# Kernel tuning notes

Measured on AMD Instinct MI355X. Metric: run time of the kernel, lower is better.

## Reference

```python
import jax, jax.numpy as jnp
import numpy as np

DIM_Q = 512
DIM_K = 512
DIM_V = 512
NUM_HEADS = 8
TEMPERATURE = 0.1
LN_EPS = 1e-5


def setup_inputs() -> dict:
    key = jax.random.key(0)
    ks = jax.random.split(key, 12)
    B, n_q, n_k = 8, 1024, 1024
    s = 0.02
    return {
        "Q": jax.random.normal(ks[0], (B, n_q, DIM_Q), jnp.float32),
        "K": jax.random.normal(ks[1], (B, n_k, DIM_K), jnp.float32),
        "mask": jnp.ones((B, n_k), dtype=bool),
        "Wq": jax.random.normal(ks[2], (DIM_Q, DIM_V), jnp.float32) * s,
        "bq": jnp.zeros((DIM_V,), jnp.float32),
        "Wk": jax.random.normal(ks[3], (DIM_K, DIM_V), jnp.float32) * s,
        "bk": jnp.zeros((DIM_V,), jnp.float32),
        "Wv": jax.random.normal(ks[4], (DIM_K, DIM_V), jnp.float32) * s,
        "bv": jnp.zeros((DIM_V,), jnp.float32),
        "Wo": jax.random.normal(ks[5], (DIM_V, DIM_V), jnp.float32) * s,
        "bo": jnp.zeros((DIM_V,), jnp.float32),
        "gamma": jnp.ones((DIM_V,), jnp.float32),
        "beta": jnp.zeros((DIM_V,), jnp.float32),
    }


def _mab(Q, K, mask, Wq, bq, Wk, bk, Wv, bv, Wo, bo, gamma, beta):
    B, n_q, _ = Q.shape
    n_k = K.shape[1]
    H = NUM_HEADS
    d_head = DIM_V // H
    # projections, split heads: [B, H, n, d_head]
    Qh = (Q @ Wq + bq).reshape(B, n_q, H, d_head).transpose(0, 2, 1, 3)
    Kh = (K @ Wk + bk).reshape(B, n_k, H, d_head).transpose(0, 2, 1, 3)
    Vh = (K @ Wv + bv).reshape(B, n_k, H, d_head).transpose(0, 2, 1, 3)
    scale = 1.0 / (np.sqrt(d_head) * TEMPERATURE)
    A = jnp.einsum("bhqd,bhkd->bhqk", Qh, Kh) * scale
    A = jnp.where(mask[:, None, None, :], A, -jnp.inf)
    A = jax.nn.softmax(A, axis=-1)
    O = jnp.einsum("bhqk,bhkd->bhqd", A, Vh)
    O = O.transpose(0, 2, 1, 3).reshape(B, n_q, DIM_V)
    # fused output FFN + residual + LN
    O = O + jax.nn.relu(O @ Wo + bo)
    mu = jnp.mean(O, axis=-1, keepdims=True)
    var = jnp.var(O, axis=-1, keepdims=True)
    return (O - mu) * jax.lax.rsqrt(var + LN_EPS) * gamma + beta


def reference(Q, K, mask, Wq, bq, Wk, bk, Wv, bv, Wo, bo, gamma, beta):
    return _mab(Q, K, mask, Wq, bq, Wk, bk, Wv, bv, Wo, bo, gamma, beta)
```

## Files before the change

kernel.cpp:

```cpp
#include <hip/hip_runtime.h>

typedef __bf16 bf16;
typedef bf16 bf16x4 __attribute__((ext_vector_type(4)));
typedef bf16 bf16x8 __attribute__((ext_vector_type(8)));
typedef float floatx4 __attribute__((ext_vector_type(4)));

#define NB 8
#define NQ 1024
#define NK 1024
#define DIM 512
#define NH 8
#define DH 64

__device__ __forceinline__ void async16(const void* g, void* l) {
    __builtin_amdgcn_global_load_lds(
        (const __attribute__((address_space(1))) unsigned int*)(unsigned long long)(g),
        (__attribute__((address_space(3))) unsigned int*)(unsigned long long)(l),
        16, 0, 0);
}

__global__ __launch_bounds__(256) void prep_fused(
    const float* __restrict__ Q, const float* __restrict__ K,
    const float* __restrict__ Wq, const float* __restrict__ Wk,
    const float* __restrict__ Wv, const float* __restrict__ Wo,
    bf16* __restrict__ Qb, bf16* __restrict__ Kb, bf16* __restrict__ Wt)
{
    __shared__ bf16 Tl[64][68];
    const int bid = blockIdx.x;
    if (bid < 4096) {
        const int i = bid * 256 + threadIdx.x;
        float4 a = ((const float4*)Q)[i];
        float4 c = ((const float4*)K)[i];
        bf16x4 qa = {(bf16)a.x, (bf16)a.y, (bf16)a.z, (bf16)a.w};
        bf16x4 ka = {(bf16)c.x, (bf16)c.y, (bf16)c.z, (bf16)c.w};
        *(bf16x4*)(Qb + (size_t)i * 4) = qa;
        *(bf16x4*)(Kb + (size_t)i * 4) = ka;
    } else {
        const int bid2 = bid - 4096;
        const int w = bid2 >> 6;
        const int bx = bid2 & 7, by = (bid2 >> 3) & 7;
        const float* W = (w == 0) ? Wq : (w == 1) ? Wk : (w == 2) ? Wv : Wo;
        bf16* out = Wt + (size_t)w * DIM * DIM;
        const int k0 = bx * 64, n0 = by * 64;
        const int tx = threadIdx.x & 15, ty = threadIdx.x >> 4;
        for (int pass = 0; pass < 4; ++pass) {
            int k = ty + pass * 16;
            float4 v = *(const float4*)&W[(size_t)(k0 + k) * DIM + n0 + tx * 4];
            Tl[tx * 4 + 0][k] = (bf16)v.x;
            Tl[tx * 4 + 1][k] = (bf16)v.y;
            Tl[tx * 4 + 2][k] = (bf16)v.z;
            Tl[tx * 4 + 3][k] = (bf16)v.w;
        }
        __syncthreads();
        for (int pass = 0; pass < 4; ++pass) {
            int n = ty + pass * 16;
            bf16x4 ov = *(const bf16x4*)&Tl[n][tx * 4];
            *(bf16x4*)&out[(size_t)(n0 + n) * DIM + k0 + tx * 4] = ov;
        }
    }
}

__global__ __launch_bounds__(256) void proj_fused(
    const bf16* __restrict__ Qb, const bf16* __restrict__ Kb,
    const bf16* __restrict__ Wt,
    const float* __restrict__ bq, const float* __restrict__ bk,
    const float* __restrict__ bv,
    bf16* __restrict__ Qp, bf16* __restrict__ Kp, bf16* __restrict__ Vpt)
{
    __shared__ __attribute__((aligned(16))) bf16 sh[24576];
    const int t = threadIdx.x;
    const int wave = t >> 6, lane = t & 63, quad = lane >> 4, l16 = lane & 15;
    const int wr = wave >> 1, wc = wave & 1;
    const int bid = blockIdx.x;
    const bool isQ = bid < 512;
    const bf16* A; const bf16* W; int m0, n0;
    if (isQ) { A = Qb; W = Wt;             m0 = (bid & 63) * 128;  n0 = (bid >> 6) * 64; }
    else     { int b2 = bid - 512;
               A = Kb; W = Wt + 512 * DIM; m0 = (b2 & 63) * 128;   n0 = (b2 >> 6) * 64; }

    const int r1 = t >> 3, s1 = t & 7;
    const int p1 = s1 ^ (r1 & 7);
    const bf16* aSrc = A + (size_t)(m0 + r1) * DIM + p1 * 8;
    const bf16* wSrc = W + (size_t)(n0 + r1) * DIM + p1 * 8;

    floatx4 acc[4][2];
    for (int i = 0; i < 4; ++i)
        for (int j = 0; j < 2; ++j) acc[i][j] = (floatx4){0.f, 0.f, 0.f, 0.f};

    #pragma unroll
    for (int j = 0; j < 4; ++j)
        async16(aSrc + (size_t)j * 32 * DIM, sh + (t + j * 256) * 8);
    #pragma unroll
    for (int j = 0; j < 2; ++j)
        async16(wSrc + (size_t)j * 32 * DIM, sh + 16384 + (t + j * 256) * 8);

    for (int kt = 0; kt < 8; ++kt) {
        __syncthreads();
        const int cur = kt & 1;
        bf16* Acur = sh + cur * 8192;
        bf16* Bcur = sh + 16384 + cur * 4096;
        if (kt < 7) {
            bf16* Anxt = sh + (1 - cur) * 8192;
            bf16* Bnxt = sh + 16384 + (1 - cur) * 4096;
            const int ko = (kt + 1) * 64;
            #pragma unroll
            for (int j = 0; j < 4; ++j)
                async16(aSrc + ko + (size_t)j * 32 * DIM, Anxt + (t + j * 256) * 8);
            #pragma unroll
            for (int j = 0; j < 2; ++j)
                async16(wSrc + ko + (size_t)j * 32 * DIM, Bnxt + (t + j * 256) * 8);
        }
        #pragma unroll
        for (int ks = 0; ks < 2; ++ks) {
            bf16x8 af[4], bfr[2];
            #pragma unroll
            for (int mi = 0; mi < 4; ++mi) {
                const int row = wr * 64 + mi * 16 + l16;
                af[mi] = *(const bf16x8*)(Acur + row * 64 + (((ks * 4 + quad) ^ (row & 7)) << 3));
            }
            #pragma unroll
            for (int ni = 0; ni < 2; ++ni) {
                const int row = wc * 32 + ni * 16 + l16;
                bfr[ni] = *(const bf16x8*)(Bcur + row * 64 + (((ks * 4 + quad) ^ (row & 7)) << 3));
            }
            #pragma unroll
            for (int mi = 0; mi < 4; ++mi)
                #pragma unroll
                for (int ni = 0; ni < 2; ++ni)
                    acc[mi][ni] = __builtin_amdgcn_mfma_f32_16x16x32_bf16(
                        af[mi], bfr[ni], acc[mi][ni], 0, 0, 0);
        }
    }

    const bool isV = (!isQ) && (n0 >= 512);
    if (!isV) {
        bf16* out = isQ ? Qp : Kp;
        const float* bias = isQ ? bq : bk;
        const float qscale = isQ ? 1.8033688f : 1.0f;
        for (int ni = 0; ni < 2; ++ni) {
            const int n = n0 + wc * 32 + ni * 16 + l16;
            const float bb = bias[n];
            const int hd = n >> 6, d = n & 63;
            for (int mi = 0; mi < 4; ++mi) {
                for (int r = 0; r < 4; ++r) {
                    const int m = m0 + wr * 64 + mi * 16 + quad * 4 + r;
                    const int b = m >> 10, q = m & 1023;
                    out[((size_t)(b * 8 + hd) * 1024 + q) * 64 + d] =
                        (bf16)((acc[mi][ni][r] + bb) * qscale);
                }
            }
        }
    } else {
        __syncthreads();
        for (int ni = 0; ni < 2; ++ni) {
            const int n = wc * 32 + ni * 16 + l16;
            const float bb = bv[n0 + n - 512];
            for (int mi = 0; mi < 4; ++mi) {
                const int mb = wr * 64 + mi * 16 + quad * 4;
                const int slot = ((mb >> 3) ^ (n & 15));
                bf16x4 pk = {(bf16)(acc[mi][ni][0] + bb), (bf16)(acc[mi][ni][1] + bb),
                             (bf16)(acc[mi][ni][2] + bb), (bf16)(acc[mi][ni][3] + bb)};
                *(bf16x4*)(sh + n * 128 + slot * 8 + (mb & 7)) = pk;
            }
        }
        __syncthreads();
        const int n = t >> 2, hf = t & 3;
        const int nv = n0 + n - 512, hd = nv >> 6, d = nv & 63;
        const int b = m0 >> 10, qb = m0 & 1023;
        bf16* dst = Vpt + ((size_t)(b * 8 + hd) * 64 + d) * 1024 + qb;
        #pragma unroll
        for (int j = 0; j < 4; ++j) {
            const int ch = hf * 4 + j;
            const int slot = ch ^ (n & 15);
            bf16x8 v8 = *(const bf16x8*)(sh + n * 128 + slot * 8);
            *(bf16x8*)(dst + ch * 8) = v8;
        }
    }
}

__global__ __launch_bounds__(256) void attn_kernel(
    const bf16* __restrict__ Qp, const bf16* __restrict__ Kp,
    const bf16* __restrict__ Vpt, const int* __restrict__ mask,
    bf16* __restrict__ Oa)
{
    const int bh = blockIdx.x & 63, qblk = blockIdx.x >> 6;
    const int b = bh >> 3, hd = bh & 7;
    const int t = threadIdx.x;
    const int wave = t >> 6, lane = t & 63, quad = lane >> 4, l16 = lane & 15;

    __shared__ __attribute__((aligned(16))) bf16 Kt[2][64 * 64];
    __shared__ __attribute__((aligned(16))) bf16 Vt[2][64 * 64];
    __shared__ __attribute__((aligned(16))) bf16 Pl[4][16 * 64];

    const bf16* Qbase = Qp + ((size_t)bh * NQ + qblk * 64 + wave * 16) * DH;
    const bf16* Kbase = Kp + (size_t)bh * NK * DH;
    const bf16* Vbase = Vpt + (size_t)bh * DH * NK;
    const int* mrow = mask + b * NK;

    bf16x8 qf[2];
    #pragma unroll
    for (int hh = 0; hh < 2; ++hh)
        qf[hh] = *(const bf16x8*)(Qbase + (size_t)l16 * DH + hh * 32 + quad * 8);

    bf16x8 onesv;
    #pragma unroll
    for (int j = 0; j < 8; ++j) onesv[j] = (bf16)1.0f;

    floatx4 o[4];
    floatx4 osum = (floatx4){0.f, 0.f, 0.f, 0.f};
    #pragma unroll
    for (int i = 0; i < 4; ++i) o[i] = (floatx4){0.f, 0.f, 0.f, 0.f};

    const int r1 = t >> 3, s1 = t & 7;
    const int p1 = s1 ^ (r1 & 7);
    const bf16* kSrc = Kbase + r1 * 64 + p1 * 8;
    const bf16* vSrc = Vbase + (size_t)r1 * 1024 + p1 * 8;

    async16(kSrc, Kt[0] + t * 8);
    async16(kSrc + 32 * 64, Kt[0] + (t + 256) * 8);
    async16(vSrc, Vt[0] + t * 8);
    async16(vSrc + (size_t)32 * 1024, Vt[0] + (t + 256) * 8);

    for (int kt = 0; kt < NK / 64; ++kt) {
        __syncthreads();
        const int cur = kt & 1;
        if (kt < NK / 64 - 1) {
            const int nxt = 1 - cur;
            async16(kSrc + (kt + 1) * 4096, Kt[nxt] + t * 8);
            async16(kSrc + (kt + 1) * 4096 + 32 * 64, Kt[nxt] + (t + 256) * 8);
            async16(vSrc + (kt + 1) * 64, Vt[nxt] + t * 8);
            async16(vSrc + (kt + 1) * 64 + (size_t)32 * 1024, Vt[nxt] + (t + 256) * 8);
        }

        bf16x8 kb[4][2];
        #pragma unroll
        for (int sub = 0; sub < 4; ++sub) {
            const int rowk = sub * 16 + l16;
            kb[sub][0] = *(const bf16x8*)(Kt[cur] + rowk * 64 + ((quad ^ (rowk & 7)) << 3));
            kb[sub][1] = *(const bf16x8*)(Kt[cur] + rowk * 64 + (((quad + 4) ^ (rowk & 7)) << 3));
        }
        floatx4 sf[4];
        __builtin_amdgcn_s_setprio(1);
        #pragma unroll
        for (int sub = 0; sub < 4; ++sub) {
            floatx4 s = {0.f, 0.f, 0.f, 0.f};
            s = __builtin_amdgcn_mfma_f32_16x16x32_bf16(kb[sub][0], qf[0], s, 0, 0, 0);
            s = __builtin_amdgcn_mfma_f32_16x16x32_bf16(kb[sub][1], qf[1], s, 0, 0, 0);
            sf[sub] = s;
        }
        __builtin_amdgcn_s_setprio(0);

        const int mv = mrow[kt * 64 + lane];
        if (!__all(mv != 0)) {
            #pragma unroll
            for (int sub = 0; sub < 4; ++sub) {
                const int4 m4 = *(const int4*)&mrow[kt * 64 + sub * 16 + quad * 4];
                if (!m4.x) sf[sub][0] = -3.0e38f;
                if (!m4.y) sf[sub][1] = -3.0e38f;
                if (!m4.z) sf[sub][2] = -3.0e38f;
                if (!m4.w) sf[sub][3] = -3.0e38f;
            }
        }
        #pragma unroll
        for (int sub = 0; sub < 4; ++sub) {
            sf[sub][0] = __builtin_amdgcn_exp2f(sf[sub][0]);
            sf[sub][1] = __builtin_amdgcn_exp2f(sf[sub][1]);
            sf[sub][2] = __builtin_amdgcn_exp2f(sf[sub][2]);
            sf[sub][3] = __builtin_amdgcn_exp2f(sf[sub][3]);
        }
        #pragma unroll
        for (int sub = 0; sub < 4; ++sub) {
            bf16x4 pk = {(bf16)sf[sub][0], (bf16)sf[sub][1],
                         (bf16)sf[sub][2], (bf16)sf[sub][3]};
            const int slot = (sub * 2 + (quad >> 1)) ^ (l16 & 7);
            *(bf16x4*)&Pl[wave][l16 * 64 + slot * 8 + (quad & 1) * 4] = pk;
        }
        bf16x8 af[2];
        #pragma unroll
        for (int hh = 0; hh < 2; ++hh) {
            const int slot = (hh * 4 + quad) ^ (l16 & 7);
            af[hh] = *(const bf16x8*)&Pl[wave][l16 * 64 + slot * 8];
        }
        __builtin_amdgcn_s_setprio(1);
        osum = __builtin_amdgcn_mfma_f32_16x16x32_bf16(af[0], onesv, osum, 0, 0, 0);
        osum = __builtin_amdgcn_mfma_f32_16x16x32_bf16(af[1], onesv, osum, 0, 0, 0);
        #pragma unroll
        for (int dsub = 0; dsub < 4; ++dsub) {
            const int rowd = dsub * 16 + l16;
            bf16x8 v0 = *(const bf16x8*)(Vt[cur] + rowd * 64 + ((quad ^ (rowd & 7)) << 3));
            bf16x8 v1 = *(const bf16x8*)(Vt[cur] + rowd * 64 + (((quad + 4) ^ (rowd & 7)) << 3));
            o[dsub] = __builtin_amdgcn_mfma_f32_16x16x32_bf16(af[0], v0, o[dsub], 0, 0, 0);
            o[dsub] = __builtin_amdgcn_mfma_f32_16x16x32_bf16(af[1], v1, o[dsub], 0, 0, 0);
        }
        __builtin_amdgcn_s_setprio(0);
    }

    float linv[4];
    #pragma unroll
    for (int r = 0; r < 4; ++r) linv[r] = 1.f / osum[r];
    for (int dsub = 0; dsub < 4; ++dsub) {
        for (int r = 0; r < 4; ++r) {
            const int q = qblk * 64 + wave * 16 + quad * 4 + r;
            const int col = hd * 64 + dsub * 16 + l16;
            Oa[((size_t)(b * NQ + q)) * DIM + col] = (bf16)(o[dsub][r] * linv[r]);
        }
    }
}

__global__ __launch_bounds__(256) void ffn_gemm(
    const bf16* __restrict__ Oa, const bf16* __restrict__ W,
    const float* __restrict__ bias, bf16* __restrict__ Yb)
{
    __shared__ __attribute__((aligned(16))) bf16 sh[24576];
    const int t = threadIdx.x;
    const int wave = t >> 6, lane = t & 63, quad = lane >> 4, l16 = lane & 15;
    const int wr = wave >> 1, wc = wave & 1;
    const int m0 = (blockIdx.x & 63) * 128, n0 = (blockIdx.x >> 6) * 64;

    const int r1 = t >> 3, s1 = t & 7;
    const int p1 = s1 ^ (r1 & 7);
    const bf16* aSrc = Oa + (size_t)(m0 + r1) * DIM + p1 * 8;
    const bf16* wSrc = W  + (size_t)(n0 + r1) * DIM + p1 * 8;

    floatx4 acc[4][2];
    for (int i = 0; i < 4; ++i)
        for (int j = 0; j < 2; ++j) acc[i][j] = (floatx4){0.f, 0.f, 0.f, 0.f};

    #pragma unroll
    for (int j = 0; j < 4; ++j)
        async16(aSrc + (size_t)j * 32 * DIM, sh + (t + j * 256) * 8);
    #pragma unroll
    for (int j = 0; j < 2; ++j)
        async16(wSrc + (size_t)j * 32 * DIM, sh + 16384 + (t + j * 256) * 8);

    for (int kt = 0; kt < 8; ++kt) {
        __syncthreads();
        const int cur = kt & 1;
        bf16* Acur = sh + cur * 8192;
        bf16* Bcur = sh + 16384 + cur * 4096;
        if (kt < 7) {
            bf16* Anxt = sh + (1 - cur) * 8192;
            bf16* Bnxt = sh + 16384 + (1 - cur) * 4096;
            const int ko = (kt + 1) * 64;
            #pragma unroll
            for (int j = 0; j < 4; ++j)
                async16(aSrc + ko + (size_t)j * 32 * DIM, Anxt + (t + j * 256) * 8);
            #pragma unroll
            for (int j = 0; j < 2; ++j)
                async16(wSrc + ko + (size_t)j * 32 * DIM, Bnxt + (t + j * 256) * 8);
        }
        #pragma unroll
        for (int ks = 0; ks < 2; ++ks) {
            bf16x8 af[4], bfr[2];
            #pragma unroll
            for (int mi = 0; mi < 4; ++mi) {
                const int row = wr * 64 + mi * 16 + l16;
                af[mi] = *(const bf16x8*)(Acur + row * 64 + (((ks * 4 + quad) ^ (row & 7)) << 3));
            }
            #pragma unroll
            for (int ni = 0; ni < 2; ++ni) {
                const int row = wc * 32 + ni * 16 + l16;
                bfr[ni] = *(const bf16x8*)(Bcur + row * 64 + (((ks * 4 + quad) ^ (row & 7)) << 3));
            }
            #pragma unroll
            for (int mi = 0; mi < 4; ++mi)
                #pragma unroll
                for (int ni = 0; ni < 2; ++ni)
                    acc[mi][ni] = __builtin_amdgcn_mfma_f32_16x16x32_bf16(
                        af[mi], bfr[ni], acc[mi][ni], 0, 0, 0);
        }
    }

    for (int ni = 0; ni < 2; ++ni) {
        const int n = n0 + wc * 32 + ni * 16 + l16;
        const float bb = bias[n];
        for (int mi = 0; mi < 4; ++mi) {
            for (int r = 0; r < 4; ++r) {
                const int m = m0 + wr * 64 + mi * 16 + quad * 4 + r;
                const float ov = (float)Oa[(size_t)m * DIM + n];
                Yb[(size_t)m * DIM + n] = (bf16)(ov + fmaxf(acc[mi][ni][r] + bb, 0.f));
            }
        }
    }
}

__global__ __launch_bounds__(256) void ln_kernel(
    const bf16* __restrict__ Y, const float* __restrict__ gamma,
    const float* __restrict__ beta, float* __restrict__ out)
{
    const int row  = blockIdx.x * 4 + (threadIdx.x >> 6);
    const int lane = threadIdx.x & 63;
    bf16x8 v = *(const bf16x8*)(Y + (size_t)row * DIM + lane * 8);
    float f[8];
    float s = 0.f, sq = 0.f;
    #pragma unroll
    for (int j = 0; j < 8; ++j) {
        f[j] = (float)v[j];
        s += f[j];
        sq += f[j] * f[j];
    }
    for (int mk = 32; mk >= 1; mk >>= 1) {
        s  += __shfl_xor(s,  mk, 64);
        sq += __shfl_xor(sq, mk, 64);
    }
    const float mu  = s * (1.f / 512.f);
    const float var = sq * (1.f / 512.f) - mu * mu;
    const float inv = rsqrtf(var + 1e-5f);
    float4 g1 = ((const float4*)gamma)[lane * 2];
    float4 g2 = ((const float4*)gamma)[lane * 2 + 1];
    float4 b1 = ((const float4*)beta)[lane * 2];
    float4 b2 = ((const float4*)beta)[lane * 2 + 1];
    float4 o1, o2;
    o1.x = (f[0] - mu) * inv * g1.x + b1.x;
    o1.y = (f[1] - mu) * inv * g1.y + b1.y;
    o1.z = (f[2] - mu) * inv * g1.z + b1.z;
    o1.w = (f[3] - mu) * inv * g1.w + b1.w;
    o2.x = (f[4] - mu) * inv * g2.x + b2.x;
    o2.y = (f[5] - mu) * inv * g2.y + b2.y;
    o2.z = (f[6] - mu) * inv * g2.z + b2.z;
    o2.w = (f[7] - mu) * inv * g2.w + b2.w;
    float* orow = out + (size_t)row * DIM;
    ((float4*)orow)[lane * 2]     = o1;
    ((float4*)orow)[lane * 2 + 1] = o2;
}

extern "C" void kernel_launch(void* const* d_in, const int* in_sizes, int n_in,
                              void* d_out, int out_size, void* d_ws, size_t ws_size,
                              hipStream_t stream) {
    const float* Q  = (const float*)d_in[0];
    const float* K  = (const float*)d_in[1];
    const int*   mask = (const int*)d_in[2];
    const float* Wq = (const float*)d_in[3];
    const float* bq = (const float*)d_in[4];
    const float* Wk = (const float*)d_in[5];
    const float* bk = (const float*)d_in[6];
    const float* Wv = (const float*)d_in[7];
    const float* bv = (const float*)d_in[8];
    const float* Wo = (const float*)d_in[9];
    const float* bo = (const float*)d_in[10];
    const float* gamma = (const float*)d_in[11];
    const float* beta  = (const float*)d_in[12];

    char* ws = (char*)d_ws;
    bf16* Wt  = (bf16*)(ws);
    bf16* Qb  = (bf16*)(ws + 2097152);
    bf16* Kb  = (bf16*)(ws + 10485760);
    bf16* Qp  = (bf16*)(ws + 18874368);
    bf16* Kp  = (bf16*)(ws + 27262976);
    bf16* Vpt = (bf16*)(ws + 35651584);
    bf16* Oa  = (bf16*)(ws + 44040192);
    bf16* Yb  = (bf16*)(ws + 52428800);
    float* out = (float*)d_out;

    prep_fused<<<4352, 256, 0, stream>>>(Q, K, Wq, Wk, Wv, Wo, Qb, Kb, Wt);
    proj_fused<<<1536, 256, 0, stream>>>(Qb, Kb, Wt, bq, bk, bv, Qp, Kp, Vpt);
    attn_kernel<<<1024, 256, 0, stream>>>(Qp, Kp, Vpt, mask, Oa);
    ffn_gemm<<<512, 256, 0, stream>>>(Oa, Wt + 3 * 262144, bo, Yb);
    ln_kernel<<<2048, 256, 0, stream>>>(Yb, gamma, beta, out);
}
```

Baseline: 165.6 us.

## Split attention waves over key columns with cross-wave output reduction

Each wave now owns a 16-key slice of every K/V tile and processes all 64 queries, instead of owning 16 queries and reading the whole tile. This takes the P matrix out of LDS and drops the ones-vector MFMA for the row sum: the probabilities stay in registers and feed 16x16x16 MFMAs, and row sums are accumulated in scalar registers. The cost is a larger register footprint (a 4x4 set of accumulators) and a multi-step cross-wave reduction of partial outputs through LDS at the end, followed by a coalesced store. Launch bounds now request 3 blocks per CU.

```diff
diff --git a/kernel.cpp b/kernel.cpp
--- a/kernel.cpp
+++ b/kernel.cpp
@@ -4,6 +4,7 @@
 typedef bf16 bf16x4 __attribute__((ext_vector_type(4)));
 typedef bf16 bf16x8 __attribute__((ext_vector_type(8)));
 typedef float floatx4 __attribute__((ext_vector_type(4)));
+typedef short short4i __attribute__((ext_vector_type(4)));
 
 #define NB 8
 #define NQ 1024
@@ -17,6 +18,19 @@
         (const __attribute__((address_space(1))) unsigned int*)(unsigned long long)(g),
         (__attribute__((address_space(3))) unsigned int*)(unsigned long long)(l),
         16, 0, 0);
+}
+
+__device__ __forceinline__ floatx4 mfma_16x16x16(bf16x4 a, bf16x4 b, floatx4 c) {
+#if __has_builtin(__builtin_amdgcn_mfma_f32_16x16x16_bf16)
+    return __builtin_amdgcn_mfma_f32_16x16x16_bf16(a, b, c, 0, 0, 0);
+#elif __has_builtin(__builtin_amdgcn_mfma_f32_16x16x16bf16_1k)
+    return __builtin_amdgcn_mfma_f32_16x16x16bf16_1k(
+        __builtin_bit_cast(short4i, a), __builtin_bit_cast(short4i, b), c, 0, 0, 0);
+#else
+    asm volatile("v_mfma_f32_16x16x16_bf16 %0, %1, %2, %0\n\ts_nop 7\n\ts_nop 7"
+                 : "+v"(c) : "v"(a), "v"(b));
+    return c;
+#endif
 }
 
 __global__ __launch_bounds__(256) void prep_fused(
@@ -178,7 +192,7 @@
     }
 }
 
-__global__ __launch_bounds__(256) void attn_kernel(
+__global__ __launch_bounds__(256, 3) void attn_kernel(
     const bf16* __restrict__ Qp, const bf16* __restrict__ Kp,
     const bf16* __restrict__ Vpt, const int* __restrict__ mask,
     bf16* __restrict__ Oa)
@@ -188,121 +202,181 @@
     const int t = threadIdx.x;
     const int wave = t >> 6, lane = t & 63, quad = lane >> 4, l16 = lane & 15;
 
-    __shared__ __attribute__((aligned(16))) bf16 Kt[2][64 * 64];
-    __shared__ __attribute__((aligned(16))) bf16 Vt[2][64 * 64];
-    __shared__ __attribute__((aligned(16))) bf16 Pl[4][16 * 64];
-
-    const bf16* Qbase = Qp + ((size_t)bh * NQ + qblk * 64 + wave * 16) * DH;
+    __shared__ __attribute__((aligned(16))) bf16 KV[16384];
+    __shared__ float Ls[4][64];
+
+    const bf16* Qbase = Qp + ((size_t)bh * NQ + qblk * 64) * DH;
     const bf16* Kbase = Kp + (size_t)bh * NK * DH;
     const bf16* Vbase = Vpt + (size_t)bh * DH * NK;
     const int* mrow = mask + b * NK;
 
-    bf16x8 qf[2];
-    #pragma unroll
-    for (int hh = 0; hh < 2; ++hh)
-        qf[hh] = *(const bf16x8*)(Qbase + (size_t)l16 * DH + hh * 32 + quad * 8);
-
-    bf16x8 onesv;
-    #pragma unroll
-    for (int j = 0; j < 8; ++j) onesv[j] = (bf16)1.0f;
-
-    floatx4 o[4];
-    floatx4 osum = (floatx4){0.f, 0.f, 0.f, 0.f};
-    #pragma unroll
-    for (int i = 0; i < 4; ++i) o[i] = (floatx4){0.f, 0.f, 0.f, 0.f};
+    bf16x8 qf[4][2];
+    #pragma unroll
+    for (int qg = 0; qg < 4; ++qg)
+        #pragma unroll
+        for (int hh = 0; hh < 2; ++hh)
+            qf[qg][hh] = *(const bf16x8*)(Qbase + (size_t)(qg * 16 + l16) * DH + hh * 32 + quad * 8);
+
+    floatx4 o[4][4];
+    float lsum[4] = {0.f, 0.f, 0.f, 0.f};
+    #pragma unroll
+    for (int i = 0; i < 4; ++i)
+        #pragma unroll
+        for (int j = 0; j < 4; ++j) o[i][j] = (floatx4){0.f, 0.f, 0.f, 0.f};
 
     const int r1 = t >> 3, s1 = t & 7;
     const int p1 = s1 ^ (r1 & 7);
     const bf16* kSrc = Kbase + r1 * 64 + p1 * 8;
     const bf16* vSrc = Vbase + (size_t)r1 * 1024 + p1 * 8;
 
-    async16(kSrc, Kt[0] + t * 8);
-    async16(kSrc + 32 * 64, Kt[0] + (t + 256) * 8);
-    async16(vSrc, Vt[0] + t * 8);
-    async16(vSrc + (size_t)32 * 1024, Vt[0] + (t + 256) * 8);
-
+    async16(kSrc, KV + t * 8);
+    async16(kSrc + 32 * 64, KV + (t + 256) * 8);
+    async16(vSrc, KV + 8192 + t * 8);
+    async16(vSrc + (size_t)32 * 1024, KV + 8192 + (t + 256) * 8);
+
+    const int rowk = wave * 16 + l16;
     for (int kt = 0; kt < NK / 64; ++kt) {
         __syncthreads();
         const int cur = kt & 1;
+        bf16* Ktc = KV + cur * 4096;
+        bf16* Vtc = KV + 8192 + cur * 4096;
         if (kt < NK / 64 - 1) {
             const int nxt = 1 - cur;
-            async16(kSrc + (kt + 1) * 4096, Kt[nxt] + t * 8);
-            async16(kSrc + (kt + 1) * 4096 + 32 * 64, Kt[nxt] + (t + 256) * 8);
-            async16(vSrc + (kt + 1) * 64, Vt[nxt] + t * 8);
-            async16(vSrc + (kt + 1) * 64 + (size_t)32 * 1024, Vt[nxt] + (t + 256) * 8);
-        }
-
-        bf16x8 kb[4][2];
-        #pragma unroll
-        for (int sub = 0; sub < 4; ++sub) {
-            const int rowk = sub * 16 + l16;
-            kb[sub][0] = *(const bf16x8*)(Kt[cur] + rowk * 64 + ((quad ^ (rowk & 7)) << 3));
-            kb[sub][1] = *(const bf16x8*)(Kt[cur] + rowk * 64 + (((quad + 4) ^ (rowk & 7)) << 3));
-        }
+            async16(kSrc + (kt + 1) * 4096, KV + nxt * 4096 + t * 8);
+            async16(kSrc + (kt + 1) * 4096 + 32 * 64, KV + nxt * 4096 + (t + 256) * 8);
+            async16(vSrc + (kt + 1) * 64, KV + 8192 + nxt * 4096 + t * 8);
+            async16(vSrc + (kt + 1) * 64 + (size_t)32 * 1024, KV + 8192 + nxt * 4096 + (t + 256) * 8);
+        }
+
+        bf16x8 kb0 = *(const bf16x8*)(Ktc + rowk * 64 + ((quad ^ (rowk & 7)) << 3));
+        bf16x8 kb1 = *(const bf16x8*)(Ktc + rowk * 64 + (((quad + 4) ^ (rowk & 7)) << 3));
+
         floatx4 sf[4];
         __builtin_amdgcn_s_setprio(1);
         #pragma unroll
-        for (int sub = 0; sub < 4; ++sub) {
+        for (int qg = 0; qg < 4; ++qg) {
             floatx4 s = {0.f, 0.f, 0.f, 0.f};
-            s = __builtin_amdgcn_mfma_f32_16x16x32_bf16(kb[sub][0], qf[0], s, 0, 0, 0);
-            s = __builtin_amdgcn_mfma_f32_16x16x32_bf16(kb[sub][1], qf[1], s, 0, 0, 0);
-            sf[sub] = s;
+            s = __builtin_amdgcn_mfma_f32_16x16x32_bf16(kb0, qf[qg][0], s, 0, 0, 0);
+            s = __builtin_amdgcn_mfma_f32_16x16x32_bf16(kb1, qf[qg][1], s, 0, 0, 0);
+            sf[qg] = s;
         }
         __builtin_amdgcn_s_setprio(0);
 
         const int mv = mrow[kt * 64 + lane];
         if (!__all(mv != 0)) {
-            #pragma unroll
-            for (int sub = 0; sub < 4; ++sub) {
-                const int4 m4 = *(const int4*)&mrow[kt * 64 + sub * 16 + quad * 4];
-                if (!m4.x) sf[sub][0] = -3.0e38f;
-                if (!m4.y) sf[sub][1] = -3.0e38f;
-                if (!m4.z) sf[sub][2] = -3.0e38f;
-                if (!m4.w) sf[sub][3] = -3.0e38f;
-            }
-        }
-        #pragma unroll
-        for (int sub = 0; sub < 4; ++sub) {
-            sf[sub][0] = __builtin_amdgcn_exp2f(sf[sub][0]);
-            sf[sub][1] = __builtin_amdgcn_exp2f(sf[sub][1]);
-            sf[sub][2] = __builtin_amdgcn_exp2f(sf[sub][2]);
-            sf[sub][3] = __builtin_amdgcn_exp2f(sf[sub][3]);
-        }
-        #pragma unroll
-        for (int sub = 0; sub < 4; ++sub) {
-            bf16x4 pk = {(bf16)sf[sub][0], (bf16)sf[sub][1],
-                         (bf16)sf[sub][2], (bf16)sf[sub][3]};
-            const int slot = (sub * 2 + (quad >> 1)) ^ (l16 & 7);
-            *(bf16x4*)&Pl[wave][l16 * 64 + slot * 8 + (quad & 1) * 4] = pk;
-        }
-        bf16x8 af[2];
-        #pragma unroll
-        for (int hh = 0; hh < 2; ++hh) {
-            const int slot = (hh * 4 + quad) ^ (l16 & 7);
-            af[hh] = *(const bf16x8*)&Pl[wave][l16 * 64 + slot * 8];
+            const int4 m4 = *(const int4*)&mrow[kt * 64 + wave * 16 + quad * 4];
+            #pragma unroll
+            for (int qg = 0; qg < 4; ++qg) {
+                if (!m4.x) sf[qg][0] = -3.0e38f;
+                if (!m4.y) sf[qg][1] = -3.0e38f;
+                if (!m4.z) sf[qg][2] = -3.0e38f;
+                if (!m4.w) sf[qg][3] = -3.0e38f;
+            }
+        }
+        bf16x4 pb[4];
+        #pragma unroll
+        for (int qg = 0; qg < 4; ++qg) {
+            const float e0 = __builtin_amdgcn_exp2f(sf[qg][0]);
+            const float e1 = __builtin_amdgcn_exp2f(sf[qg][1]);
+            const float e2 = __builtin_amdgcn_exp2f(sf[qg][2]);
+            const float e3 = __builtin_amdgcn_exp2f(sf[qg][3]);
+            lsum[qg] += (e0 + e1) + (e2 + e3);
+            pb[qg] = (bf16x4){(bf16)e0, (bf16)e1, (bf16)e2, (bf16)e3};
         }
         __builtin_amdgcn_s_setprio(1);
-        osum = __builtin_amdgcn_mfma_f32_16x16x32_bf16(af[0], onesv, osum, 0, 0, 0);
-        osum = __builtin_amdgcn_mfma_f32_16x16x32_bf16(af[1], onesv, osum, 0, 0, 0);
         #pragma unroll
         for (int dsub = 0; dsub < 4; ++dsub) {
-            const int rowd = dsub * 16 + l16;
-            bf16x8 v0 = *(const bf16x8*)(Vt[cur] + rowd * 64 + ((quad ^ (rowd & 7)) << 3));
-            bf16x8 v1 = *(const bf16x8*)(Vt[cur] + rowd * 64 + (((quad + 4) ^ (rowd & 7)) << 3));
-            o[dsub] = __builtin_amdgcn_mfma_f32_16x16x32_bf16(af[0], v0, o[dsub], 0, 0, 0);
-            o[dsub] = __builtin_amdgcn_mfma_f32_16x16x32_bf16(af[1], v1, o[dsub], 0, 0, 0);
+            const int d = dsub * 16 + l16;
+            bf16x4 av = *(const bf16x4*)(Vtc + d * 64 +
+                                         (((wave * 4 + quad) ^ ((d & 7) << 1)) << 2));
+            #pragma unroll
+            for (int qg = 0; qg < 4; ++qg)
+                o[dsub][qg] = mfma_16x16x16(av, pb[qg], o[dsub][qg]);
         }
         __builtin_amdgcn_s_setprio(0);
     }
 
-    float linv[4];
-    #pragma unroll
-    for (int r = 0; r < 4; ++r) linv[r] = 1.f / osum[r];
-    for (int dsub = 0; dsub < 4; ++dsub) {
-        for (int r = 0; r < 4; ++r) {
-            const int q = qblk * 64 + wave * 16 + quad * 4 + r;
-            const int col = hd * 64 + dsub * 16 + l16;
-            Oa[((size_t)(b * NQ + q)) * DIM + col] = (bf16)(o[dsub][r] * linv[r]);
+    __syncthreads();
+    float* scr = (float*)KV;
+
+    #pragma unroll
+    for (int qg = 0; qg < 4; ++qg) {
+        lsum[qg] += __shfl_xor(lsum[qg], 16, 64);
+        lsum[qg] += __shfl_xor(lsum[qg], 32, 64);
+    }
+    if (quad == 0)
+        #pragma unroll
+        for (int qg = 0; qg < 4; ++qg) Ls[wave][qg * 16 + l16] = lsum[qg];
+
+    {
+        const int rA = (wave + 1) & 3, rB = (wave + 2) & 3;
+        float* sA = scr + (rA * 2 + 0) * 1024;
+        float* sB = scr + (rB * 2 + 1) * 1024;
+        #pragma unroll
+        for (int qg = 0; qg < 4; ++qg) {
+            const int q = qg * 16 + l16, cs = quad ^ (l16 & 3);
+            *(floatx4*)(sA + q * 16 + cs * 4) = o[rA][qg];
+            *(floatx4*)(sB + q * 16 + cs * 4) = o[rB][qg];
+        }
+    }
+    __syncthreads();
+    float inv[4];
+    #pragma unroll
+    for (int qg = 0; qg < 4; ++qg) {
+        const int q = qg * 16 + l16;
+        inv[qg] = 1.f / (Ls[0][q] + Ls[1][q] + Ls[2][q] + Ls[3][q]);
+    }
+    {
+        float* sA = scr + (wave * 2 + 0) * 1024;
+        float* sB = scr + (wave * 2 + 1) * 1024;
+        #pragma unroll
+        for (int qg = 0; qg < 4; ++qg) {
+            const int q = qg * 16 + l16, cs = quad ^ (l16 & 3);
+            o[wave][qg] += *(const floatx4*)(sA + q * 16 + cs * 4);
+            o[wave][qg] += *(const floatx4*)(sB + q * 16 + cs * 4);
+        }
+    }
+    __syncthreads();
+    {
+        const int rC = (wave + 3) & 3;
+        float* sC = scr + (rC * 2 + 0) * 1024;
+        #pragma unroll
+        for (int qg = 0; qg < 4; ++qg) {
+            const int q = qg * 16 + l16, cs = quad ^ (l16 & 3);
+            *(floatx4*)(sC + q * 16 + cs * 4) = o[rC][qg];
+        }
+    }
+    __syncthreads();
+    {
+        float* sC = scr + (wave * 2 + 0) * 1024;
+        #pragma unroll
+        for (int qg = 0; qg < 4; ++qg) {
+            const int q = qg * 16 + l16, cs = quad ^ (l16 & 3);
+            o[wave][qg] += *(const floatx4*)(sC + q * 16 + cs * 4);
+        }
+    }
+    __syncthreads();
+    {
+        bf16* Ot = KV;
+        #pragma unroll
+        for (int qg = 0; qg < 4; ++qg) {
+            const int q = qg * 16 + l16;
+            const int chunk = (wave * 2 + (quad >> 1)) ^ (q & 7);
+            bf16x4 pk = {(bf16)(o[wave][qg][0] * inv[qg]), (bf16)(o[wave][qg][1] * inv[qg]),
+                         (bf16)(o[wave][qg][2] * inv[qg]), (bf16)(o[wave][qg][3] * inv[qg])};
+            *(bf16x4*)(Ot + q * 64 + chunk * 8 + (quad & 1) * 4) = pk;
+        }
+    }
+    __syncthreads();
+    {
+        const bf16* Ot = KV;
+        const int q = t >> 2, cp = t & 3;
+        bf16* orow = Oa + ((size_t)(b * NQ + qblk * 64 + q)) * DIM + hd * 64;
+        #pragma unroll
+        for (int i = 0; i < 2; ++i) {
+            const int c = cp * 2 + i;
+            bf16x8 v = *(const bf16x8*)(Ot + q * 64 + (c ^ (q & 7)) * 8);
+            *(bf16x8*)(orow + c * 8) = v;
         }
     }
 }
```

Result: slower. 461.6 us (+178.7%).

## Feed softmax probabilities directly into transposed PV MFMA and stage output through LDS

Applied to the files above, without the earlier changes.

The attention PV product is reformulated as O^T = V^T·P^T using 16x16x16 MFMAs, so the exponentiated scores held in registers can be used directly as the B operand, with no per-wave LDS round-trip. The row sum is now accumulated with scalar adds plus cross-lane shuffles instead of an extra MFMA against a ones vector. The transposed output tile is written to LDS and then stored with coalesced 16-byte global writes instead of scattered 2-byte stores. This trades twice as many smaller MFMAs and narrower V reads for less LDS traffic and better store coalescing.

```diff
diff --git a/kernel.cpp b/kernel.cpp
--- a/kernel.cpp
+++ b/kernel.cpp
@@ -4,6 +4,7 @@
 typedef bf16 bf16x4 __attribute__((ext_vector_type(4)));
 typedef bf16 bf16x8 __attribute__((ext_vector_type(8)));
 typedef float floatx4 __attribute__((ext_vector_type(4)));
+typedef short short4i __attribute__((ext_vector_type(4)));
 
 #define NB 8
 #define NQ 1024
@@ -17,6 +18,19 @@
         (const __attribute__((address_space(1))) unsigned int*)(unsigned long long)(g),
         (__attribute__((address_space(3))) unsigned int*)(unsigned long long)(l),
         16, 0, 0);
+}
+
+__device__ __forceinline__ floatx4 mfma_16x16x16(bf16x4 a, bf16x4 b, floatx4 c) {
+#if __has_builtin(__builtin_amdgcn_mfma_f32_16x16x16_bf16)
+    return __builtin_amdgcn_mfma_f32_16x16x16_bf16(a, b, c, 0, 0, 0);
+#elif __has_builtin(__builtin_amdgcn_mfma_f32_16x16x16bf16_1k)
+    return __builtin_amdgcn_mfma_f32_16x16x16bf16_1k(
+        __builtin_bit_cast(short4i, a), __builtin_bit_cast(short4i, b), c, 0, 0, 0);
+#else
+    asm volatile("v_mfma_f32_16x16x16_bf16 %0, %1, %2, %0\n\ts_nop 7\n\ts_nop 7"
+                 : "+v"(c) : "v"(a), "v"(b));
+    return c;
+#endif
 }
 
 __global__ __launch_bounds__(256) void prep_fused(
@@ -190,7 +204,7 @@
 
     __shared__ __attribute__((aligned(16))) bf16 Kt[2][64 * 64];
     __shared__ __attribute__((aligned(16))) bf16 Vt[2][64 * 64];
-    __shared__ __attribute__((aligned(16))) bf16 Pl[4][16 * 64];
+    __shared__ __attribute__((aligned(16))) bf16 Ot[64 * 64];
 
     const bf16* Qbase = Qp + ((size_t)bh * NQ + qblk * 64 + wave * 16) * DH;
     const bf16* Kbase = Kp + (size_t)bh * NK * DH;
@@ -202,12 +216,8 @@
     for (int hh = 0; hh < 2; ++hh)
         qf[hh] = *(const bf16x8*)(Qbase + (size_t)l16 * DH + hh * 32 + quad * 8);
 
-    bf16x8 onesv;
-    #pragma unroll
-    for (int j = 0; j < 8; ++j) onesv[j] = (bf16)1.0f;
-
     floatx4 o[4];
-    floatx4 osum = (floatx4){0.f, 0.f, 0.f, 0.f};
+    float lsum = 0.f;
     #pragma unroll
     for (int i = 0; i < 4; ++i) o[i] = (floatx4){0.f, 0.f, 0.f, 0.f};
 
@@ -261,48 +271,54 @@
                 if (!m4.w) sf[sub][3] = -3.0e38f;
             }
         }
+        bf16x4 pb[4];
         #pragma unroll
         for (int sub = 0; sub < 4; ++sub) {
-            sf[sub][0] = __builtin_amdgcn_exp2f(sf[sub][0]);
-            sf[sub][1] = __builtin_amdgcn_exp2f(sf[sub][1]);
-            sf[sub][2] = __builtin_amdgcn_exp2f(sf[sub][2]);
-            sf[sub][3] = __builtin_amdgcn_exp2f(sf[sub][3]);
-        }
+            const float e0 = __builtin_amdgcn_exp2f(sf[sub][0]);
+            const float e1 = __builtin_amdgcn_exp2f(sf[sub][1]);
+            const float e2 = __builtin_amdgcn_exp2f(sf[sub][2]);
+            const float e3 = __builtin_amdgcn_exp2f(sf[sub][3]);
+            lsum += (e0 + e1) + (e2 + e3);
+            pb[sub] = (bf16x4){(bf16)e0, (bf16)e1, (bf16)e2, (bf16)e3};
+        }
+        __builtin_amdgcn_s_setprio(1);
         #pragma unroll
         for (int sub = 0; sub < 4; ++sub) {
-            bf16x4 pk = {(bf16)sf[sub][0], (bf16)sf[sub][1],
-                         (bf16)sf[sub][2], (bf16)sf[sub][3]};
-            const int slot = (sub * 2 + (quad >> 1)) ^ (l16 & 7);
-            *(bf16x4*)&Pl[wave][l16 * 64 + slot * 8 + (quad & 1) * 4] = pk;
-        }
-        bf16x8 af[2];
-        #pragma unroll
-        for (int hh = 0; hh < 2; ++hh) {
-            const int slot = (hh * 4 + quad) ^ (l16 & 7);
-            af[hh] = *(const bf16x8*)&Pl[wave][l16 * 64 + slot * 8];
-        }
-        __builtin_amdgcn_s_setprio(1);
-        osum = __builtin_amdgcn_mfma_f32_16x16x32_bf16(af[0], onesv, osum, 0, 0, 0);
-        osum = __builtin_amdgcn_mfma_f32_16x16x32_bf16(af[1], onesv, osum, 0, 0, 0);
-        #pragma unroll
-        for (int dsub = 0; dsub < 4; ++dsub) {
-            const int rowd = dsub * 16 + l16;
-            bf16x8 v0 = *(const bf16x8*)(Vt[cur] + rowd * 64 + ((quad ^ (rowd & 7)) << 3));
-            bf16x8 v1 = *(const bf16x8*)(Vt[cur] + rowd * 64 + (((quad + 4) ^ (rowd & 7)) << 3));
-            o[dsub] = __builtin_amdgcn_mfma_f32_16x16x32_bf16(af[0], v0, o[dsub], 0, 0, 0);
-            o[dsub] = __builtin_amdgcn_mfma_f32_16x16x32_bf16(af[1], v1, o[dsub], 0, 0, 0);
+            #pragma unroll
+            for (int dg = 0; dg < 4; ++dg) {
+                const int d = dg * 16 + l16;
+                bf16x4 av = *(const bf16x4*)(Vt[cur] + d * 64 +
+                    (((sub * 2 + (quad >> 1)) ^ (l16 & 7)) << 3) + (quad & 1) * 4);
+                o[dg] = mfma_16x16x16(av, pb[sub], o[dg]);
+            }
         }
         __builtin_amdgcn_s_setprio(0);
     }
 
-    float linv[4];
-    #pragma unroll
-    for (int r = 0; r < 4; ++r) linv[r] = 1.f / osum[r];
-    for (int dsub = 0; dsub < 4; ++dsub) {
-        for (int r = 0; r < 4; ++r) {
-            const int q = qblk * 64 + wave * 16 + quad * 4 + r;
-            const int col = hd * 64 + dsub * 16 + l16;
-            Oa[((size_t)(b * NQ + q)) * DIM + col] = (bf16)(o[dsub][r] * linv[r]);
+    lsum += __shfl_xor(lsum, 16, 64);
+    lsum += __shfl_xor(lsum, 32, 64);
+    const float inv = 1.f / lsum;
+
+    {
+        const int q = wave * 16 + l16;
+        #pragma unroll
+        for (int dg = 0; dg < 4; ++dg) {
+            const int ch = dg * 2 + (quad >> 1);
+            const int slot = ch ^ (l16 & 7);
+            bf16x4 pk = {(bf16)(o[dg][0] * inv), (bf16)(o[dg][1] * inv),
+                         (bf16)(o[dg][2] * inv), (bf16)(o[dg][3] * inv)};
+            *(bf16x4*)(Ot + q * 64 + slot * 8 + (quad & 1) * 4) = pk;
+        }
+    }
+    __syncthreads();
+    {
+        const int q = t >> 2, cp = t & 3;
+        bf16* orow = Oa + ((size_t)(b * NQ + qblk * 64 + q)) * DIM + hd * 64;
+        #pragma unroll
+        for (int j = 0; j < 2; ++j) {
+            const int c = cp * 2 + j;
+            bf16x8 v = *(const bf16x8*)(Ot + q * 64 + (c ^ (q & 7)) * 8);
+            *(bf16x8*)(orow + c * 8) = v;
         }
     }
 }
```

Result: slower. 170.5 us (+3.0%).
